# Optimization experiments

Hardware: AMD Instinct MI355X
Metric: run time of the kernel (lower is better)

Reference implementation:

```python
import jax, jax.numpy as jnp
import numpy as np

EPS = 1e-5
NEG_SLOPE = 0.2

def _bn(x, g, be, m, v):
    # inference-mode BatchNorm1d over the channel (last) dim
    return (x - m) * jax.lax.rsqrt(v + EPS) * g + be

def _lrelu(x):
    return jnp.where(x >= 0, x, NEG_SLOPE * x)

def setup_inputs() -> dict:
    key = jax.random.key(0)
    ks = jax.random.split(key, 32)
    B, N, M = 2, 65536, 16
    C_RAW, C_IN, C_RO, C_NB, C_OUT = 10, 32, 32, 64, 64
    i = iter(range(32))
    def nrm(shape, s=1.0):
        return jax.random.normal(ks[next(i)], shape, dtype=jnp.float32) * s
    def pos(shape):
        return jax.random.uniform(ks[next(i)], shape, dtype=jnp.float32)
    inp = {}
    inp['feature'] = nrm((B, N, C_IN))
    inp['raw_nb_fea'] = nrm((B, N, M, C_RAW))
    inp['neighbors_idx'] = jax.random.randint(ks[next(i)], (B, N, M), 0, N, dtype=jnp.int32)
    inp['w_raw'] = nrm((C_RAW, C_RO), 0.3); inp['b_raw'] = nrm((C_RO,), 0.1)
    inp['g_raw'] = pos((C_RO,)); inp['be_raw'] = nrm((C_RO,), 0.1)
    inp['m_raw'] = nrm((C_RO,), 0.1); inp['v_raw'] = pos((C_RO,))
    inp['w_nb'] = nrm((C_NB, C_NB), 0.15); inp['b_nb'] = nrm((C_NB,), 0.1)
    inp['g_nb'] = pos((C_NB,)); inp['be_nb'] = nrm((C_NB,), 0.1)
    inp['m_nb'] = nrm((C_NB,), 0.1); inp['v_nb'] = pos((C_NB,))
    inp['w_attn'] = nrm((C_NB, C_NB), 0.15)
    inp['w_out'] = nrm((C_NB, C_OUT), 0.15); inp['b_out'] = nrm((C_OUT,), 0.1)
    inp['g_out'] = pos((C_OUT,)); inp['be_out'] = nrm((C_OUT,), 0.1)
    inp['m_out'] = nrm((C_OUT,), 0.1); inp['v_out'] = pos((C_OUT,))
    inp['w_sc'] = nrm((C_IN, C_OUT), 0.3); inp['b_sc'] = nrm((C_OUT,), 0.1)
    inp['g_sc'] = pos((C_OUT,)); inp['be_sc'] = nrm((C_OUT,), 0.1)
    inp['m_sc'] = nrm((C_OUT,), 0.1); inp['v_sc'] = pos((C_OUT,))
    return inp

def reference(feature, raw_nb_fea, neighbors_idx,
              w_raw, b_raw, g_raw, be_raw, m_raw, v_raw,
              w_nb, b_nb, g_nb, be_nb, m_nb, v_nb,
              w_attn,
              w_out, b_out, g_out, be_out, m_out, v_out,
              w_sc, b_sc, g_sc, be_sc, m_sc, v_sc):
    B = feature.shape[0]
    # mlp_raw_neighbor_fea: (B,N,M,10) -> (B,N,M,32)
    raw_mlp = _lrelu(_bn(raw_nb_fea @ w_raw + b_raw, g_raw, be_raw, m_raw, v_raw))
    # index_points: gather neighbor features (B,N,M,C_in)
    b_idx = jnp.arange(B)[:, None, None]
    nb_fea = feature[b_idx, neighbors_idx]  # (B,N,M,32)
    cat = jnp.concatenate([nb_fea, raw_mlp], axis=3)  # (B,N,M,64)
    # mlp_neighbor_fea
    h = _lrelu(_bn(cat @ w_nb + b_nb, g_nb, be_nb, m_nb, v_nb))  # (B,N,M,64)
    # attention pooling over neighbor dim M
    attn = jax.nn.softmax(h @ w_attn, axis=2)
    pooled = jnp.sum(attn * h, axis=2)  # (B,N,64)
    # out + shortcut, leaky_relu
    out = _bn(pooled @ w_out + b_out, g_out, be_out, m_out, v_out)
    sc = _bn(feature @ w_sc + b_sc, g_sc, be_sc, m_sc, v_sc)
    return _lrelu(sc + out)
```

## Files before the change

kernel.cpp:

```cpp
#include <hip/hip_runtime.h>
#include <hip/hip_bf16.h>

typedef unsigned short u16;
typedef unsigned int u32;
typedef __attribute__((ext_vector_type(8))) short short8;
typedef __attribute__((ext_vector_type(4))) float f32x4;

typedef float __attribute__((may_alias)) f32a;
typedef __attribute__((ext_vector_type(2))) float f32x2_t;
typedef f32x2_t __attribute__((may_alias)) f32x2a;
typedef __attribute__((ext_vector_type(4))) float f32x4_t;
typedef f32x4_t __attribute__((may_alias)) f32x4a;
typedef __attribute__((ext_vector_type(2))) u32 u32x2_t;
typedef u32x2_t __attribute__((may_alias)) u32x2a;

#define NSLOPE 0.2f
#define BNEPS  1e-5f

union U8 { short8 s; u16 u[8]; u32 w[4]; };

__device__ __forceinline__ u16 f2bf_scalar(float f) {
    union { float f; u32 i; } x; x.f = f;
    u32 u = x.i + 0x7FFFu + ((x.i >> 16) & 1u);
    return (u16)(u >> 16);
}

__device__ __forceinline__ u32 cvt2(float a, float b) {
#if __has_builtin(__builtin_amdgcn_cvt_pk_bf16_f32)
    auto p = __builtin_amdgcn_cvt_pk_bf16_f32(a, b);
    u32 w; __builtin_memcpy(&w, &p, sizeof(u32));
    return w;
#else
    return (u32)f2bf_scalar(a) | ((u32)f2bf_scalar(b) << 16);
#endif
}
__device__ __forceinline__ u16 cvt1(float a) { return (u16)cvt2(a, a); }

__device__ __forceinline__ float lrelu(float x) { return fmaxf(x, NSLOPE * x); }

__device__ __forceinline__ short8 load_bfrag(const void* W, int K, int Cn, int ks, int nt,
                                             int q, int t) {
    U8 x;
#pragma unroll
    for (int j = 0; j < 8; ++j) {
        int k = ks * 32 + q * 8 + j;
        x.u[j] = (k < K) ? f2bf_scalar(((const f32a*)W)[(size_t)k * Cn + nt * 16 + t]) : (u16)0;
    }
    return x.s;
}

__device__ __forceinline__ short8 lds_afrag(const u16* buf, int row, int ks, int q) {
    const u16* cp = buf + row * 68 + ks * 32 + q * 8;
    u32x2a a = *(const u32x2a*)cp;
    u32x2a b = *(const u32x2a*)(cp + 4);
    U8 x; x.w[0] = a.x; x.w[1] = a.y; x.w[2] = b.x; x.w[3] = b.y;
    return x.s;
}

__device__ __forceinline__ float ldf(const void* p, size_t i) { return ((const f32a*)p)[i]; }

#define MFMA(a, b, c) __builtin_amdgcn_mfma_f32_16x16x32_bf16((a), (b), (c), 0, 0, 0)

__global__ __launch_bounds__(256, 3) void lfa_kernel(
    const void* __restrict__ feat,
    const void* __restrict__ rawf,
    const int*  __restrict__ nbidx,
    const void* __restrict__ w_raw,
    const void* __restrict__ b_raw, const void* __restrict__ g_raw,
    const void* __restrict__ be_raw, const void* __restrict__ m_raw,
    const void* __restrict__ v_raw,
    const void* __restrict__ w_nb,
    const void* __restrict__ b_nb, const void* __restrict__ g_nb,
    const void* __restrict__ be_nb, const void* __restrict__ m_nb,
    const void* __restrict__ v_nb,
    const void* __restrict__ w_attn,
    const void* __restrict__ w_out,
    const void* __restrict__ b_out, const void* __restrict__ g_out,
    const void* __restrict__ be_out, const void* __restrict__ m_out,
    const void* __restrict__ v_out,
    const void* __restrict__ w_sc,
    const void* __restrict__ b_sc, const void* __restrict__ g_sc,
    const void* __restrict__ be_sc, const void* __restrict__ m_sc,
    const void* __restrict__ v_sc,
    float* __restrict__ outp)
{
    __shared__ __align__(16) u16 s_cat[4][16 * 68];
    __shared__ __align__(16) u16 s_h[4][16 * 68];
    __shared__ __align__(16) u16 s_pool[4][16 * 68];
    __shared__ float2 s_pr_raw[32];
    __shared__ float2 s_pr_nb[64];
    __shared__ float2 s_pr_out[64];
    __shared__ float2 s_pr_sc[64];

    const int tid  = threadIdx.x;
    const int lane = tid & 63;
    const int wv   = tid >> 6;
    const int t    = lane & 15;
    const int q    = lane >> 4;

    if (tid < 64) {
        int c = tid;
        float s = ldf(g_nb, c) * rsqrtf(ldf(v_nb, c) + BNEPS);
        s_pr_nb[c] = make_float2(s, (ldf(b_nb, c) - ldf(m_nb, c)) * s + ldf(be_nb, c));
    } else if (tid < 128) {
        int c = tid - 64;
        float s = ldf(g_out, c) * rsqrtf(ldf(v_out, c) + BNEPS);
        s_pr_out[c] = make_float2(s, (ldf(b_out, c) - ldf(m_out, c)) * s + ldf(be_out, c));
    } else if (tid < 192) {
        int c = tid - 128;
        float s = ldf(g_sc, c) * rsqrtf(ldf(v_sc, c) + BNEPS);
        s_pr_sc[c] = make_float2(s, (ldf(b_sc, c) - ldf(m_sc, c)) * s + ldf(be_sc, c));
    } else if (tid < 224) {
        int c = tid - 192;
        float s = ldf(g_raw, c) * rsqrtf(ldf(v_raw, c) + BNEPS);
        s_pr_raw[c] = make_float2(s, (ldf(b_raw, c) - ldf(m_raw, c)) * s + ldf(be_raw, c));
    }
    __syncthreads();

    short8 wraw[2], wnb[2][4], watt[2][4];
#pragma unroll
    for (int nt = 0; nt < 2; ++nt) wraw[nt] = load_bfrag(w_raw, 10, 32, 0, nt, q, t);
#pragma unroll
    for (int ks = 0; ks < 2; ++ks)
#pragma unroll
        for (int nt = 0; nt < 4; ++nt) {
            wnb[ks][nt]  = load_bfrag(w_nb,   64, 64, ks, nt, q, t);
            watt[ks][nt] = load_bfrag(w_attn, 64, 64, ks, nt, q, t);
        }

    u16* catw  = &s_cat[wv][0];
    u16* hw    = &s_h[wv][0];
    u16* poolw = &s_pool[wv][0];

    const f32x4 zf = {0.f, 0.f, 0.f, 0.f};
    const int g  = blockIdx.x * 4 + wv;
    const int P0 = g * 16;
    const int bb = P0 >> 16;
    const size_t fb = (size_t)bb << 16;

    const int m_ = lane >> 2;
    const int pc = lane & 3;

    const int*  nbp  = nbidx + P0 * 16 + m_;
    const f32a* rawp = (const f32a*)rawf + (size_t)P0 * 160 + (size_t)t * 10;
    const float* fpb = (const float*)feat;

    auto load_gather = [&](int ix, f32x4& a, f32x4& b) {
        const float* fp = fpb + (fb + (size_t)ix) * 32 + pc * 8;
        a = *(const f32x4a*)fp;
        b = *(const f32x4a*)(fp + 4);
    };
    auto load_raw = [&](int p, f32x4& a, f32x4& b) {
        const f32a* rp = rawp + (size_t)p * 160;
        f32x2a r01 = *(const f32x2a*)rp;
        f32x2a r23 = *(const f32x2a*)(rp + 2);
        f32x2a r45 = *(const f32x2a*)(rp + 4);
        f32x2a r67 = *(const f32x2a*)(rp + 6);
        f32x2a r89 = *(const f32x2a*)(rp + 8);
        float q0 = (q == 0) ? 1.f : 0.f;
        float q1 = (q == 1) ? 1.f : 0.f;
        a.x = q0 * r01.x + q1 * r89.x;
        a.y = q0 * r01.y + q1 * r89.y;
        a.z = q0 * r23.x; a.w = q0 * r23.y;
        b.x = q0 * r45.x; b.y = q0 * r45.y;
        b.z = q0 * r67.x; b.w = q0 * r67.y;
    };

    int ixA = nbp[0];
    int ixB = nbp[16];
    f32x4 ga0, ga1, ra0, ra1;
    load_gather(ixA, ga0, ga1);
    load_raw(0, ra0, ra1);

#pragma unroll 1
    for (int p = 0; p < 16; ++p) {
        const int pn  = (p + 1 < 16) ? p + 1 : 15;
        const int pnn = (p + 2 < 16) ? p + 2 : 15;
        f32x4 gb0, gb1, rb0, rb1;
        load_gather(ixB, gb0, gb1);
        load_raw(pn, rb0, rb1);
        int ixC = nbp[pnn * 16];

        {
            u32x2a lo, hi;
            lo.x = cvt2(ga0.x, ga0.y); lo.y = cvt2(ga0.z, ga0.w);
            hi.x = cvt2(ga1.x, ga1.y); hi.y = cvt2(ga1.z, ga1.w);
            *(u32x2a*)(catw + m_ * 68 + pc * 8)     = lo;
            *(u32x2a*)(catw + m_ * 68 + pc * 8 + 4) = hi;
        }
        {
            U8 au;
            au.w[0] = cvt2(ra0.x, ra0.y); au.w[1] = cvt2(ra0.z, ra0.w);
            au.w[2] = cvt2(ra1.x, ra1.y); au.w[3] = cvt2(ra1.z, ra1.w);
            short8 ar = au.s;
            f32x4 racc[2];
            racc[0] = MFMA(ar, wraw[0], zf);
            racc[1] = MFMA(ar, wraw[1], zf);
#pragma unroll
            for (int nt = 0; nt < 2; ++nt) {
                int c = nt * 16 + t;
                float2 pr = s_pr_raw[c];
#pragma unroll
                for (int r = 0; r < 4; ++r) {
                    float x = lrelu(fmaf(racc[nt][r], pr.x, pr.y));
                    catw[(q * 4 + r) * 68 + 32 + c] = cvt1(x);
                }
            }
        }

        short8 a0 = lds_afrag(catw, t, 0, q);
        short8 a1 = lds_afrag(catw, t, 1, q);
        float hv[4][4];
#pragma unroll
        for (int nt = 0; nt < 4; ++nt) {
            f32x4 a = zf;
            a = MFMA(a0, wnb[0][nt], a);
            a = MFMA(a1, wnb[1][nt], a);
            float2 pr = s_pr_nb[nt * 16 + t];
#pragma unroll
            for (int r = 0; r < 4; ++r) {
                hv[nt][r] = lrelu(fmaf(a[r], pr.x, pr.y));
                hw[(q * 4 + r) * 68 + nt * 16 + t] = cvt1(hv[nt][r]);
            }
        }

        short8 h0 = lds_afrag(hw, t, 0, q);
        short8 h1 = lds_afrag(hw, t, 1, q);
        float pooled[4];
#pragma unroll
        for (int nt = 0; nt < 4; ++nt) {
            f32x4 s = zf;
            s = MFMA(h0, watt[0][nt], s);
            s = MFMA(h1, watt[1][nt], s);
            float num = 0.f, den = 0.f;
#pragma unroll
            for (int r = 0; r < 4; ++r) {
                float e = __expf(s[r]);
                num += e * hv[nt][r];
                den += e;
            }
            num += __shfl_xor(num, 16); den += __shfl_xor(den, 16);
            num += __shfl_xor(num, 32); den += __shfl_xor(den, 32);
            pooled[nt] = num / den;
        }
        float pv = (q == 0) ? pooled[0] : (q == 1) ? pooled[1]
                 : (q == 2) ? pooled[2] : pooled[3];
        poolw[p * 68 + q * 16 + t] = cvt1(pv);

        ga0 = gb0; ga1 = gb1; ra0 = rb0; ra1 = rb1; ixB = ixC;
    }

    short8 wout[2][4], wsc[4];
#pragma unroll
    for (int ks = 0; ks < 2; ++ks)
#pragma unroll
        for (int nt = 0; nt < 4; ++nt) wout[ks][nt] = load_bfrag(w_out, 64, 64, ks, nt, q, t);
#pragma unroll
    for (int nt = 0; nt < 4; ++nt) wsc[nt] = load_bfrag(w_sc, 32, 64, 0, nt, q, t);

    short8 pf0 = lds_afrag(poolw, t, 0, q);
    short8 pf1 = lds_afrag(poolw, t, 1, q);
    U8 sxu;
    {
        const float* fp = fpb + (size_t)(P0 + t) * 32 + q * 8;
        f32x4a v0 = *(const f32x4a*)fp;
        f32x4a v1 = *(const f32x4a*)(fp + 4);
        sxu.w[0] = cvt2(v0.x, v0.y); sxu.w[1] = cvt2(v0.z, v0.w);
        sxu.w[2] = cvt2(v1.x, v1.y); sxu.w[3] = cvt2(v1.z, v1.w);
    }
    short8 scf = sxu.s;
#pragma unroll
    for (int nt = 0; nt < 4; ++nt) {
        f32x4 oa = zf;
        oa = MFMA(pf0, wout[0][nt], oa);
        oa = MFMA(pf1, wout[1][nt], oa);
        f32x4 sa = MFMA(scf, wsc[nt], zf);
        float2 po = s_pr_out[nt * 16 + t];
        float2 ps = s_pr_sc[nt * 16 + t];
#pragma unroll
        for (int r = 0; r < 4; ++r) {
            float o  = fmaf(oa[r], po.x, po.y);
            float s2 = fmaf(sa[r], ps.x, ps.y);
            outp[(size_t)(P0 + q * 4 + r) * 64 + nt * 16 + t] = lrelu(o + s2);
        }
    }
}

extern "C" void kernel_launch(void* const* d_in, const int* in_sizes, int n_in,
                              void* d_out, int out_size, void* d_ws, size_t ws_size,
                              hipStream_t stream) {
    hipLaunchKernelGGL(lfa_kernel, dim3(2048), dim3(256), 0, stream,
                       d_in[0], d_in[1], (const int*)d_in[2],
                       d_in[3], d_in[4], d_in[5], d_in[6], d_in[7], d_in[8],
                       d_in[9], d_in[10], d_in[11], d_in[12], d_in[13], d_in[14],
                       d_in[15],
                       d_in[16], d_in[17], d_in[18], d_in[19], d_in[20], d_in[21],
                       d_in[22], d_in[23], d_in[24], d_in[25], d_in[26], d_in[27],
                       (float*)d_out);
}
```

Before: 294.0 us.

## Fold BN scales into weights, stage MLP weights in swizzled LDS, raise occupancy

```diff
diff --git a/kernel.cpp b/kernel.cpp
--- a/kernel.cpp
+++ b/kernel.cpp
@@ -13,9 +13,11 @@
 typedef f32x4_t __attribute__((may_alias)) f32x4a;
 typedef __attribute__((ext_vector_type(2))) u32 u32x2_t;
 typedef u32x2_t __attribute__((may_alias)) u32x2a;
+typedef short8 __attribute__((may_alias)) short8a;
 
 #define NSLOPE 0.2f
 #define BNEPS  1e-5f
+#define LOG2E  1.4426950408889634f
 
 union U8 { short8 s; u16 u[8]; u32 w[4]; };
 
@@ -38,13 +40,23 @@
 
 __device__ __forceinline__ float lrelu(float x) { return fmaxf(x, NSLOPE * x); }
 
+__device__ __forceinline__ float fexp2(float x) {
+#if __has_builtin(__builtin_amdgcn_exp2f)
+    return __builtin_amdgcn_exp2f(x);
+#else
+    return exp2f(x);
+#endif
+}
+
+__device__ __forceinline__ float ldf(const void* p, size_t i) { return ((const f32a*)p)[i]; }
+
 __device__ __forceinline__ short8 load_bfrag(const void* W, int K, int Cn, int ks, int nt,
-                                             int q, int t) {
+                                             int q, int t, float scale) {
     U8 x;
 #pragma unroll
     for (int j = 0; j < 8; ++j) {
         int k = ks * 32 + q * 8 + j;
-        x.u[j] = (k < K) ? f2bf_scalar(((const f32a*)W)[(size_t)k * Cn + nt * 16 + t]) : (u16)0;
+        x.u[j] = (k < K) ? f2bf_scalar(ldf(W, (size_t)k * Cn + nt * 16 + t) * scale) : (u16)0;
     }
     return x.s;
 }
@@ -57,11 +69,14 @@
     return x.s;
 }
 
-__device__ __forceinline__ float ldf(const void* p, size_t i) { return ((const f32a*)p)[i]; }
+__device__ __forceinline__ short8 lds_wfrag(const u16* w, int n, int ks, int q) {
+    int slot = ((ks << 2) | q) ^ (n & 7);
+    return *(const short8a*)(w + (n << 6) + (slot << 3));
+}
 
 #define MFMA(a, b, c) __builtin_amdgcn_mfma_f32_16x16x32_bf16((a), (b), (c), 0, 0, 0)
 
-__global__ __launch_bounds__(256, 3) void lfa_kernel(
+__global__ __launch_bounds__(256, 4) void lfa_kernel(
     const void* __restrict__ feat,
     const void* __restrict__ rawf,
     const int*  __restrict__ nbidx,
@@ -85,8 +100,9 @@
     float* __restrict__ outp)
 {
     __shared__ __align__(16) u16 s_cat[4][16 * 68];
-    __shared__ __align__(16) u16 s_h[4][16 * 68];
     __shared__ __align__(16) u16 s_pool[4][16 * 68];
+    __shared__ __align__(16) u16 s_wnbT[64 * 64];
+    __shared__ __align__(16) u16 s_wattT[64 * 64];
     __shared__ float2 s_pr_raw[32];
     __shared__ float2 s_pr_nb[64];
     __shared__ float2 s_pr_out[64];
@@ -117,19 +133,27 @@
     }
     __syncthreads();
 
-    short8 wraw[2], wnb[2][4], watt[2][4];
-#pragma unroll
-    for (int nt = 0; nt < 2; ++nt) wraw[nt] = load_bfrag(w_raw, 10, 32, 0, nt, q, t);
-#pragma unroll
-    for (int ks = 0; ks < 2; ++ks)
-#pragma unroll
-        for (int nt = 0; nt < 4; ++nt) {
-            wnb[ks][nt]  = load_bfrag(w_nb,   64, 64, ks, nt, q, t);
-            watt[ks][nt] = load_bfrag(w_attn, 64, 64, ks, nt, q, t);
-        }
+#pragma unroll 4
+    for (int idx = tid; idx < 64 * 64; idx += 256) {
+        int n = idx & 63, k = idx >> 6;
+        int off = (n << 6) | (((k >> 3) ^ (n & 7)) << 3) | (k & 7);
+        s_wnbT[off]  = f2bf_scalar(ldf(w_nb,   (size_t)k * 64 + n) * s_pr_nb[n].x);
+        s_wattT[off] = f2bf_scalar(ldf(w_attn, (size_t)k * 64 + n) * LOG2E);
+    }
+    __syncthreads();
+
+    short8 wraw[2];
+    float bias_raw[2], bias_nb[4];
+#pragma unroll
+    for (int nt = 0; nt < 2; ++nt) {
+        float2 pr = s_pr_raw[nt * 16 + t];
+        wraw[nt] = load_bfrag(w_raw, 10, 32, 0, nt, q, t, pr.x);
+        bias_raw[nt] = pr.y;
+    }
+#pragma unroll
+    for (int nt = 0; nt < 4; ++nt) bias_nb[nt] = s_pr_nb[nt * 16 + t].y;
 
     u16* catw  = &s_cat[wv][0];
-    u16* hw    = &s_h[wv][0];
     u16* poolw = &s_pool[wv][0];
 
     const f32x4 zf = {0.f, 0.f, 0.f, 0.f};
@@ -194,15 +218,16 @@
             au.w[2] = cvt2(ra1.x, ra1.y); au.w[3] = cvt2(ra1.z, ra1.w);
             short8 ar = au.s;
             f32x4 racc[2];
-            racc[0] = MFMA(ar, wraw[0], zf);
-            racc[1] = MFMA(ar, wraw[1], zf);
+            racc[0] = MFMA(ar, wraw[0],
+                           ((f32x4){bias_raw[0], bias_raw[0], bias_raw[0], bias_raw[0]}));
+            racc[1] = MFMA(ar, wraw[1],
+                           ((f32x4){bias_raw[1], bias_raw[1], bias_raw[1], bias_raw[1]}));
 #pragma unroll
             for (int nt = 0; nt < 2; ++nt) {
                 int c = nt * 16 + t;
-                float2 pr = s_pr_raw[c];
 #pragma unroll
                 for (int r = 0; r < 4; ++r) {
-                    float x = lrelu(fmaf(racc[nt][r], pr.x, pr.y));
+                    float x = lrelu(racc[nt][r]);
                     catw[(q * 4 + r) * 68 + 32 + c] = cvt1(x);
                 }
             }
@@ -213,29 +238,34 @@
         float hv[4][4];
 #pragma unroll
         for (int nt = 0; nt < 4; ++nt) {
-            f32x4 a = zf;
-            a = MFMA(a0, wnb[0][nt], a);
-            a = MFMA(a1, wnb[1][nt], a);
-            float2 pr = s_pr_nb[nt * 16 + t];
+            int n = nt * 16 + t;
+            short8 b0 = lds_wfrag(s_wnbT, n, 0, q);
+            short8 b1 = lds_wfrag(s_wnbT, n, 1, q);
+            f32x4 a = {bias_nb[nt], bias_nb[nt], bias_nb[nt], bias_nb[nt]};
+            a = MFMA(a0, b0, a);
+            a = MFMA(a1, b1, a);
 #pragma unroll
             for (int r = 0; r < 4; ++r) {
-                hv[nt][r] = lrelu(fmaf(a[r], pr.x, pr.y));
-                hw[(q * 4 + r) * 68 + nt * 16 + t] = cvt1(hv[nt][r]);
+                hv[nt][r] = lrelu(a[r]);
+                catw[(q * 4 + r) * 68 + nt * 16 + t] = cvt1(hv[nt][r]);
             }
         }
 
-        short8 h0 = lds_afrag(hw, t, 0, q);
-        short8 h1 = lds_afrag(hw, t, 1, q);
+        short8 h0 = lds_afrag(catw, t, 0, q);
+        short8 h1 = lds_afrag(catw, t, 1, q);
         float pooled[4];
 #pragma unroll
         for (int nt = 0; nt < 4; ++nt) {
+            int n = nt * 16 + t;
+            short8 b0 = lds_wfrag(s_wattT, n, 0, q);
+            short8 b1 = lds_wfrag(s_wattT, n, 1, q);
             f32x4 s = zf;
-            s = MFMA(h0, watt[0][nt], s);
-            s = MFMA(h1, watt[1][nt], s);
+            s = MFMA(h0, b0, s);
+            s = MFMA(h1, b1, s);
             float num = 0.f, den = 0.f;
 #pragma unroll
             for (int r = 0; r < 4; ++r) {
-                float e = __expf(s[r]);
+                float e = fexp2(s[r]);
                 num += e * hv[nt][r];
                 den += e;
             }
@@ -251,12 +281,17 @@
     }
 
     short8 wout[2][4], wsc[4];
-#pragma unroll
-    for (int ks = 0; ks < 2; ++ks)
-#pragma unroll
-        for (int nt = 0; nt < 4; ++nt) wout[ks][nt] = load_bfrag(w_out, 64, 64, ks, nt, q, t);
-#pragma unroll
-    for (int nt = 0; nt < 4; ++nt) wsc[nt] = load_bfrag(w_sc, 32, 64, 0, nt, q, t);
+    float bias_os[4];
+#pragma unroll
+    for (int nt = 0; nt < 4; ++nt) {
+        float2 po = s_pr_out[nt * 16 + t];
+        float2 ps = s_pr_sc[nt * 16 + t];
+        bias_os[nt] = po.y + ps.y;
+#pragma unroll
+        for (int ks = 0; ks < 2; ++ks)
+            wout[ks][nt] = load_bfrag(w_out, 64, 64, ks, nt, q, t, po.x);
+        wsc[nt] = load_bfrag(w_sc, 32, 64, 0, nt, q, t, ps.x);
+    }
 
     short8 pf0 = lds_afrag(poolw, t, 0, q);
     short8 pf1 = lds_afrag(poolw, t, 1, q);
@@ -271,18 +306,13 @@
     short8 scf = sxu.s;
 #pragma unroll
     for (int nt = 0; nt < 4; ++nt) {
-        f32x4 oa = zf;
+        f32x4 oa = {bias_os[nt], bias_os[nt], bias_os[nt], bias_os[nt]};
         oa = MFMA(pf0, wout[0][nt], oa);
         oa = MFMA(pf1, wout[1][nt], oa);
         f32x4 sa = MFMA(scf, wsc[nt], zf);
-        float2 po = s_pr_out[nt * 16 + t];
-        float2 ps = s_pr_sc[nt * 16 + t];
-#pragma unroll
-        for (int r = 0; r < 4; ++r) {
-            float o  = fmaf(oa[r], po.x, po.y);
-            float s2 = fmaf(sa[r], ps.x, ps.y);
-            outp[(size_t)(P0 + q * 4 + r) * 64 + nt * 16 + t] = lrelu(o + s2);
-        }
+#pragma unroll
+        for (int r = 0; r < 4; ++r)
+            outp[(size_t)(P0 + q * 4 + r) * 64 + nt * 16 + t] = lrelu(oa[r] + sa[r]);
     }
 }
 
```

New measurement: 380.1 us. 1.29x slower.
